# Performance work log

Measured on AMD Instinct MI355X. Metric: run time of the kernel, lower is better.

The kernel has to match this reference:

```python
import jax, jax.numpy as jnp
import numpy as np

N_NODES = 50000
N_EDGES = 1600000
IN_CH = 128
OUT_CH = 128


def setup_inputs() -> dict:
    key = jax.random.key(0)
    k1, k2, k3, k4, k5 = jax.random.split(key, 5)
    x = jax.random.normal(k1, (N_NODES, IN_CH), dtype=jnp.float32)
    # edge_index[0] = destination (row), edge_index[1] = source (col)
    edge_index = jax.random.randint(k2, (2, N_EDGES), 0, N_NODES, dtype=jnp.int64)
    # Linear parameters (PyTorch default init: U(-1/sqrt(fan_in), 1/sqrt(fan_in)))
    bound = 1.0 / np.sqrt(IN_CH)
    W = jax.random.uniform(k3, (OUT_CH, IN_CH), dtype=jnp.float32, minval=-bound, maxval=bound)
    b = jax.random.uniform(k4, (OUT_CH,), dtype=jnp.float32, minval=-bound, maxval=bound)
    return {"x": x, "edge_index": edge_index, "W": W, "b": b}


def reference(x, edge_index, W, b) -> jnp.ndarray:
    # Linear projection: h = x @ W^T + b  -> [N, OUT_CH]
    h = jnp.einsum("nd,od->no", x, W) + b
    # spmm sum aggregation: out[dst] = sum_{edges e: dst(e)=dst} h[src(e)]
    dst = edge_index[0]
    src = edge_index[1]
    out = jax.ops.segment_sum(h[src], dst, num_segments=N_NODES)
    return out
```

## Files before the change

kernel.cpp:

```cpp
#include <hip/hip_runtime.h>

constexpr int N  = 50000;
constexpr int E  = 1600000;
constexpr int CH = 128;

constexpr int BSZ  = 64;
constexpr int NB   = (N + BSZ - 1) / BSZ;
constexpr int CAP  = 2560;
constexpr int PBLK = 256;
constexpr int EPB  = E / PBLK;
constexpr int GEMM_BLOCKS = N / 16;

constexpr size_t H_OFF     = 0;
constexpr size_t H_SZ      = (size_t)N * CH * 2;
constexpr size_t PAIRS_OFF = H_OFF + H_SZ;
constexpr size_t PAIRS_SZ  = (size_t)NB * CAP * 4;
constexpr size_t GCUR_OFF  = PAIRS_OFF + PAIRS_SZ;
constexpr size_t GCUR_SZ   = 3328;
constexpr size_t REQUIRED  = GCUR_OFF + GCUR_SZ;
constexpr size_t FB_REQUIRED = H_SZ;

static __device__ __forceinline__ ushort f2bf(float f) {
    unsigned u = __float_as_uint(f);
    return (ushort)((u + 0x7fffu + ((u >> 16) & 1u)) >> 16);
}
static __device__ __forceinline__ float bf_lo(unsigned u) { return __uint_as_float(u << 16); }
static __device__ __forceinline__ float bf_hi(unsigned u) { return __uint_as_float(u & 0xffff0000u); }

typedef __attribute__((ext_vector_type(8))) short bf16x8;
typedef __attribute__((ext_vector_type(4))) float f32x4;

static __device__ __forceinline__ void gemm_body(int gb, int tid,
                                                 const float* __restrict__ x,
                                                 const float* __restrict__ W,
                                                 const float* __restrict__ bias,
                                                 ushort* __restrict__ h) {
    const int m    = tid & 15;
    const int q    = (tid >> 4) & 3;
    const int wave = tid >> 6;
    const int r0   = gb * 16;
    const int c0   = wave * 32;

    const float* xrow = x + (size_t)(r0 + m) * CH + q * 8;
    const float* wr0  = W + (size_t)(c0 + m) * CH + q * 8;
    const float* wr1  = wr0 + 16 * CH;

    f32x4 acc0 = {0.f, 0.f, 0.f, 0.f};
    f32x4 acc1 = {0.f, 0.f, 0.f, 0.f};

#pragma unroll
    for (int kc = 0; kc < CH; kc += 32) {
        float4 xa = *(const float4*)(xrow + kc);
        float4 xb = *(const float4*)(xrow + kc + 4);
        float4 wa0 = *(const float4*)(wr0 + kc);
        float4 wb0 = *(const float4*)(wr0 + kc + 4);
        float4 wa1 = *(const float4*)(wr1 + kc);
        float4 wb1 = *(const float4*)(wr1 + kc + 4);
        bf16x8 a, b0, b1;
        a[0] = (short)f2bf(xa.x); a[1] = (short)f2bf(xa.y);
        a[2] = (short)f2bf(xa.z); a[3] = (short)f2bf(xa.w);
        a[4] = (short)f2bf(xb.x); a[5] = (short)f2bf(xb.y);
        a[6] = (short)f2bf(xb.z); a[7] = (short)f2bf(xb.w);
        b0[0] = (short)f2bf(wa0.x); b0[1] = (short)f2bf(wa0.y);
        b0[2] = (short)f2bf(wa0.z); b0[3] = (short)f2bf(wa0.w);
        b0[4] = (short)f2bf(wb0.x); b0[5] = (short)f2bf(wb0.y);
        b0[6] = (short)f2bf(wb0.z); b0[7] = (short)f2bf(wb0.w);
        b1[0] = (short)f2bf(wa1.x); b1[1] = (short)f2bf(wa1.y);
        b1[2] = (short)f2bf(wa1.z); b1[3] = (short)f2bf(wa1.w);
        b1[4] = (short)f2bf(wb1.x); b1[5] = (short)f2bf(wb1.y);
        b1[6] = (short)f2bf(wb1.z); b1[7] = (short)f2bf(wb1.w);
        acc0 = __builtin_amdgcn_mfma_f32_16x16x32_bf16(a, b0, acc0, 0, 0, 0);
        acc1 = __builtin_amdgcn_mfma_f32_16x16x32_bf16(a, b1, acc1, 0, 0, 0);
    }

    const int col0 = c0 + m;
    const float bb0 = bias[col0];
    const float bb1 = bias[col0 + 16];
#pragma unroll
    for (int r = 0; r < 4; r++) {
        size_t row = (size_t)(r0 + q * 4 + r) * CH;
        h[row + col0]      = f2bf(acc0[r] + bb0);
        h[row + col0 + 16] = f2bf(acc1[r] + bb1);
    }
}

__global__ __launch_bounds__(256) void gemm_and_scatter(const float* __restrict__ x,
                                                        const float* __restrict__ W,
                                                        const float* __restrict__ bias,
                                                        ushort* __restrict__ h,
                                                        const int* __restrict__ ei,
                                                        int* __restrict__ gcur,
                                                        unsigned* __restrict__ pairs) {
    __shared__ unsigned raw[EPB];
    __shared__ ushort   srt16[EPB];
    __shared__ int cnt[NB];
    __shared__ int lstart[NB];
    __shared__ int gpos[NB];
    __shared__ int cur[NB];
    __shared__ int ssum[256];
    const int bid = blockIdx.x;
    const int tid = threadIdx.x;

    if (bid >= PBLK) {
        gemm_body(bid - PBLK, tid, x, W, bias, h);
        return;
    }

    const int k = bid;
    const int* dp = ei + k * EPB;
    const int* sp = ei + E + k * EPB;

    for (int j = tid; j < NB; j += 256) cnt[j] = 0;
    for (int i = tid; i < EPB; i += 256) {
        int d = dp[i], s = sp[i];
        raw[i] = ((unsigned)(d >> 6) << 22) | ((unsigned)(d & (BSZ - 1)) << 16) | (unsigned)s;
    }
    __syncthreads();

    for (int i = tid; i < EPB; i += 256) atomicAdd(&cnt[raw[i] >> 22], 1);
    __syncthreads();

    for (int j = tid; j < NB; j += 256) {
        int c = cnt[j];
        gpos[j] = j * CAP + (c ? atomicAdd(&gcur[j], c) : 0);
    }

    {
        const int base = tid * 4;
        int s = 0;
#pragma unroll
        for (int i = 0; i < 4; i++) { int j = base + i; if (j < NB) s += cnt[j]; }
        ssum[tid] = s;
        __syncthreads();
        for (int o = 1; o < 256; o <<= 1) {
            int u = (tid >= o) ? ssum[tid - o] : 0;
            __syncthreads();
            ssum[tid] += u;
            __syncthreads();
        }
        int run = ssum[tid] - s;
#pragma unroll
        for (int i = 0; i < 4; i++) {
            int j = base + i;
            if (j < NB) { lstart[j] = run; cur[j] = run; run += cnt[j]; }
        }
    }
    __syncthreads();

    for (int i = tid; i < EPB; i += 256) {
        int p = atomicAdd(&cur[raw[i] >> 22], 1);
        srt16[p] = (ushort)i;
    }
    __syncthreads();

    for (int i = tid; i < EPB; i += 256) {
        unsigned w = raw[srt16[i]];
        int bkt = w >> 22;
        int gdst = gpos[bkt] + (i - lstart[bkt]);
        if (gdst < (bkt + 1) * CAP)
            pairs[gdst] = w;
    }
}

__global__ __launch_bounds__(512) void agg_fused(const ushort* __restrict__ h,
                                                 const unsigned* __restrict__ pairs,
                                                 const int* __restrict__ gcur,
                                                 float* __restrict__ out) {
    __shared__ unsigned raw[CAP];
    __shared__ ushort   srt[CAP];
    __shared__ int hist[BSZ], offs[BSZ], cur[BSZ];
    const int b = blockIdx.x, t = threadIdx.x;
    const int cnt = min(gcur[b], CAP);
    const int wave = t >> 6;
    const int lane = t & 63;
    const int quarter = lane >> 4;
    const int cq      = lane & 15;

    const unsigned* slab = pairs + (size_t)b * CAP;
    for (int i = t; i < cnt; i += 512) raw[i] = slab[i];
    if (t < BSZ) hist[t] = 0;
    __syncthreads();
    for (int i = t; i < cnt; i += 512) atomicAdd(&hist[(raw[i] >> 16) & (BSZ - 1)], 1);
    __syncthreads();
    int v = (t < BSZ) ? hist[t] : 0;
    if (t < BSZ) offs[t] = v;
    __syncthreads();
    for (int o = 1; o < BSZ; o <<= 1) {
        int u = 0;
        if (t < BSZ && t >= o) u = offs[t - o];
        __syncthreads();
        if (t < BSZ) offs[t] += u;
        __syncthreads();
    }
    if (t < BSZ) { int excl = offs[t] - v; offs[t] = excl; cur[t] = excl; }
    __syncthreads();
    for (int i = t; i < cnt; i += 512) {
        unsigned w = raw[i];
        int p = atomicAdd(&cur[(w >> 16) & (BSZ - 1)], 1);
        srt[p] = (ushort)(w & 0xffffu);
    }
    __syncthreads();

    const ushort* hp = h + (size_t)cq * 8;

#pragma unroll
    for (int j = 0; j < 8; j++) {
        const int nl = wave * 8 + j;
        const int st = offs[nl];
        const int c  = hist[nl];
        float a0 = 0.f, a1 = 0.f, a2 = 0.f, a3 = 0.f;
        float a4 = 0.f, a5 = 0.f, a6 = 0.f, a7 = 0.f;
        int i = 0;
        for (; i + 16 <= c; i += 16) {
            const int e0 = st + i + quarter;
            int s0 = srt[e0];
            int s1 = srt[e0 + 4];
            int s2 = srt[e0 + 8];
            int s3 = srt[e0 + 12];
            uint4 v0 = *(const uint4*)(hp + (size_t)s0 * CH);
            uint4 v1 = *(const uint4*)(hp + (size_t)s1 * CH);
            uint4 v2 = *(const uint4*)(hp + (size_t)s2 * CH);
            uint4 v3 = *(const uint4*)(hp + (size_t)s3 * CH);
            a0 += bf_lo(v0.x); a1 += bf_hi(v0.x); a2 += bf_lo(v0.y); a3 += bf_hi(v0.y);
            a4 += bf_lo(v0.z); a5 += bf_hi(v0.z); a6 += bf_lo(v0.w); a7 += bf_hi(v0.w);
            a0 += bf_lo(v1.x); a1 += bf_hi(v1.x); a2 += bf_lo(v1.y); a3 += bf_hi(v1.y);
            a4 += bf_lo(v1.z); a5 += bf_hi(v1.z); a6 += bf_lo(v1.w); a7 += bf_hi(v1.w);
            a0 += bf_lo(v2.x); a1 += bf_hi(v2.x); a2 += bf_lo(v2.y); a3 += bf_hi(v2.y);
            a4 += bf_lo(v2.z); a5 += bf_hi(v2.z); a6 += bf_lo(v2.w); a7 += bf_hi(v2.w);
            a0 += bf_lo(v3.x); a1 += bf_hi(v3.x); a2 += bf_lo(v3.y); a3 += bf_hi(v3.y);
            a4 += bf_lo(v3.z); a5 += bf_hi(v3.z); a6 += bf_lo(v3.w); a7 += bf_hi(v3.w);
        }
        for (; i < c; i += 4) {
            if (i + quarter < c) {
                int s = srt[st + i + quarter];
                uint4 vv = *(const uint4*)(hp + (size_t)s * CH);
                a0 += bf_lo(vv.x); a1 += bf_hi(vv.x); a2 += bf_lo(vv.y); a3 += bf_hi(vv.y);
                a4 += bf_lo(vv.z); a5 += bf_hi(vv.z); a6 += bf_lo(vv.w); a7 += bf_hi(vv.w);
            }
        }
        a0 += __shfl_xor(a0, 16); a0 += __shfl_xor(a0, 32);
        a1 += __shfl_xor(a1, 16); a1 += __shfl_xor(a1, 32);
        a2 += __shfl_xor(a2, 16); a2 += __shfl_xor(a2, 32);
        a3 += __shfl_xor(a3, 16); a3 += __shfl_xor(a3, 32);
        a4 += __shfl_xor(a4, 16); a4 += __shfl_xor(a4, 32);
        a5 += __shfl_xor(a5, 16); a5 += __shfl_xor(a5, 32);
        a6 += __shfl_xor(a6, 16); a6 += __shfl_xor(a6, 32);
        a7 += __shfl_xor(a7, 16); a7 += __shfl_xor(a7, 32);
        const int n = b * BSZ + nl;
        if (quarter == 0 && n < N) {
            float* op = out + (size_t)n * CH + cq * 8;
            *(float4*)(op)     = make_float4(a0, a1, a2, a3);
            *(float4*)(op + 4) = make_float4(a4, a5, a6, a7);
        }
    }
}

__global__ __launch_bounds__(256) void gemm_only(const float* __restrict__ x,
                                                 const float* __restrict__ W,
                                                 const float* __restrict__ bias,
                                                 ushort* __restrict__ h) {
    gemm_body(blockIdx.x, threadIdx.x, x, W, bias, h);
}

__global__ void atomic_agg(const ushort* __restrict__ h, const int* __restrict__ ei,
                           float* __restrict__ out) {
    int tid = blockIdx.x * blockDim.x + threadIdx.x;
    int e  = tid >> 5;
    int cg = (tid & 31) * 4;
    if (e < E) {
        int d = ei[e];
        int s = ei[E + e];
        ushort4 v = *(const ushort4*)(h + (size_t)s * CH + cg);
        float* o = out + (size_t)d * CH + cg;
        atomicAdd(o + 0, __uint_as_float((unsigned)v.x << 16));
        atomicAdd(o + 1, __uint_as_float((unsigned)v.y << 16));
        atomicAdd(o + 2, __uint_as_float((unsigned)v.z << 16));
        atomicAdd(o + 3, __uint_as_float((unsigned)v.w << 16));
    }
}

extern "C" void kernel_launch(void* const* d_in, const int* in_sizes, int n_in,
                              void* d_out, int out_size, void* d_ws, size_t ws_size,
                              hipStream_t stream) {
    const float* x  = (const float*)d_in[0];
    const int*   ei = (const int*)d_in[1];
    const float* W  = (const float*)d_in[2];
    const float* b  = (const float*)d_in[3];
    float* out = (float*)d_out;

    char* ws = (char*)d_ws;
    ushort* h = (ushort*)(ws + H_OFF);

    if (ws_size >= REQUIRED) {
        unsigned* pairs = (unsigned*)(ws + PAIRS_OFF);
        int*      gcur  = (int*)(ws + GCUR_OFF);

        hipMemsetAsync(gcur, 0, NB * sizeof(int), stream);
        gemm_and_scatter<<<PBLK + GEMM_BLOCKS, 256, 0, stream>>>(x, W, b, h, ei, gcur, pairs);
        agg_fused<<<NB, 512, 0, stream>>>(h, pairs, gcur, out);
    } else if (ws_size >= FB_REQUIRED) {
        gemm_only<<<GEMM_BLOCKS, 256, 0, stream>>>(x, W, b, h);
        hipMemsetAsync(out, 0, (size_t)out_size * sizeof(float), stream);
        int total = E * 32;
        atomic_agg<<<(total + 255) / 256, 256, 0, stream>>>(h, ei, out);
    }
}
```

Measured before the change: 180.6 us.

## Pad per-node edge lists with zero sentinel row and gather eight rows per step

The aggregation kernel now rounds each node's edge count up to a multiple of 32 and fills the padding with a sentinel index that points at an extra all-zero row appended to h. This removes the remainder loop and its branches, and lets each quarter-wave issue eight independent gathers per iteration to raise memory-level parallelism. The cost is wasted gathers of the zero row, which average about 16 padded slots per node. Separately, both kernels fold histogram counting into the load loop and replace barrier-heavy shared-memory scans with wave shuffle scans.

```diff
diff --git a/kernel.cpp b/kernel.cpp
--- a/kernel.cpp
+++ b/kernel.cpp
@@ -7,12 +7,13 @@
 constexpr int BSZ  = 64;
 constexpr int NB   = (N + BSZ - 1) / BSZ;
 constexpr int CAP  = 2560;
+constexpr int SRTCAP = CAP + BSZ * 31 + 64;
 constexpr int PBLK = 256;
 constexpr int EPB  = E / PBLK;
 constexpr int GEMM_BLOCKS = N / 16;
 
 constexpr size_t H_OFF     = 0;
-constexpr size_t H_SZ      = (size_t)N * CH * 2;
+constexpr size_t H_SZ      = (size_t)(N + 1) * CH * 2;
 constexpr size_t PAIRS_OFF = H_OFF + H_SZ;
 constexpr size_t PAIRS_SZ  = (size_t)NB * CAP * 4;
 constexpr size_t GCUR_OFF  = PAIRS_OFF + PAIRS_SZ;
@@ -97,7 +98,7 @@
     __shared__ int lstart[NB];
     __shared__ int gpos[NB];
     __shared__ int cur[NB];
-    __shared__ int ssum[256];
+    __shared__ int wsum[4];
     const int bid = blockIdx.x;
     const int tid = threadIdx.x;
 
@@ -110,14 +111,16 @@
     const int* dp = ei + k * EPB;
     const int* sp = ei + E + k * EPB;
 
+    if (bid == 0 && tid < 64) ((unsigned*)(h + (size_t)N * CH))[tid] = 0u;
+
     for (int j = tid; j < NB; j += 256) cnt[j] = 0;
+    __syncthreads();
     for (int i = tid; i < EPB; i += 256) {
         int d = dp[i], s = sp[i];
-        raw[i] = ((unsigned)(d >> 6) << 22) | ((unsigned)(d & (BSZ - 1)) << 16) | (unsigned)s;
-    }
-    __syncthreads();
-
-    for (int i = tid; i < EPB; i += 256) atomicAdd(&cnt[raw[i] >> 22], 1);
+        unsigned w = ((unsigned)(d >> 6) << 22) | ((unsigned)(d & (BSZ - 1)) << 16) | (unsigned)s;
+        raw[i] = w;
+        atomicAdd(&cnt[w >> 22], 1);
+    }
     __syncthreads();
 
     for (int j = tid; j < NB; j += 256) {
@@ -130,15 +133,18 @@
         int s = 0;
 #pragma unroll
         for (int i = 0; i < 4; i++) { int j = base + i; if (j < NB) s += cnt[j]; }
-        ssum[tid] = s;
+        const int lane = tid & 63;
+        const int wid  = tid >> 6;
+        int incl = s;
+#pragma unroll
+        for (int o = 1; o < 64; o <<= 1) {
+            int u = __shfl_up(incl, o);
+            if (lane >= o) incl += u;
+        }
+        if (lane == 63) wsum[wid] = incl;
         __syncthreads();
-        for (int o = 1; o < 256; o <<= 1) {
-            int u = (tid >= o) ? ssum[tid - o] : 0;
-            __syncthreads();
-            ssum[tid] += u;
-            __syncthreads();
-        }
-        int run = ssum[tid] - s;
+        int run = incl - s;
+        for (int w = 0; w < wid; w++) run += wsum[w];
 #pragma unroll
         for (int i = 0; i < 4; i++) {
             int j = base + i;
@@ -167,8 +173,8 @@
                                                  const int* __restrict__ gcur,
                                                  float* __restrict__ out) {
     __shared__ unsigned raw[CAP];
-    __shared__ ushort   srt[CAP];
-    __shared__ int hist[BSZ], offs[BSZ], cur[BSZ];
+    __shared__ ushort   srt[SRTCAP];
+    __shared__ int hist[BSZ], offs[BSZ], cur[BSZ], cpad[BSZ];
     const int b = blockIdx.x, t = threadIdx.x;
     const int cnt = min(gcur[b], CAP);
     const int wave = t >> 6;
@@ -176,23 +182,34 @@
     const int quarter = lane >> 4;
     const int cq      = lane & 15;
 
+    if (t < BSZ) hist[t] = 0;
+    __syncthreads();
+
     const unsigned* slab = pairs + (size_t)b * CAP;
-    for (int i = t; i < cnt; i += 512) raw[i] = slab[i];
-    if (t < BSZ) hist[t] = 0;
-    __syncthreads();
-    for (int i = t; i < cnt; i += 512) atomicAdd(&hist[(raw[i] >> 16) & (BSZ - 1)], 1);
-    __syncthreads();
-    int v = (t < BSZ) ? hist[t] : 0;
-    if (t < BSZ) offs[t] = v;
-    __syncthreads();
-    for (int o = 1; o < BSZ; o <<= 1) {
-        int u = 0;
-        if (t < BSZ && t >= o) u = offs[t - o];
-        __syncthreads();
-        if (t < BSZ) offs[t] += u;
-        __syncthreads();
-    }
-    if (t < BSZ) { int excl = offs[t] - v; offs[t] = excl; cur[t] = excl; }
+    for (int i = t; i < cnt; i += 512) {
+        unsigned w = slab[i];
+        raw[i] = w;
+        atomicAdd(&hist[(w >> 16) & (BSZ - 1)], 1);
+    }
+    __syncthreads();
+
+    if (t < BSZ) {
+        int c  = hist[t];
+        int cp = (c + 31) & ~31;
+        int incl = cp;
+#pragma unroll
+        for (int o = 1; o < 64; o <<= 1) {
+            int u = __shfl_up(incl, o);
+            if (lane >= o) incl += u;
+        }
+        offs[t] = incl - cp;
+        cur[t]  = incl - cp;
+        cpad[t] = cp;
+    }
+    __syncthreads();
+
+    const int tot = offs[BSZ - 1] + cpad[BSZ - 1];
+    for (int i = t; i < tot; i += 512) srt[i] = (ushort)N;
     __syncthreads();
     for (int i = t; i < cnt; i += 512) {
         unsigned w = raw[i];
@@ -203,24 +220,31 @@
 
     const ushort* hp = h + (size_t)cq * 8;
 
-#pragma unroll
+#pragma unroll 1
     for (int j = 0; j < 8; j++) {
         const int nl = wave * 8 + j;
         const int st = offs[nl];
-        const int c  = hist[nl];
+        const int cp = cpad[nl];
         float a0 = 0.f, a1 = 0.f, a2 = 0.f, a3 = 0.f;
         float a4 = 0.f, a5 = 0.f, a6 = 0.f, a7 = 0.f;
-        int i = 0;
-        for (; i + 16 <= c; i += 16) {
+        for (int i = 0; i < cp; i += 32) {
             const int e0 = st + i + quarter;
-            int s0 = srt[e0];
-            int s1 = srt[e0 + 4];
-            int s2 = srt[e0 + 8];
-            int s3 = srt[e0 + 12];
+            const int s0 = srt[e0];
+            const int s1 = srt[e0 + 4];
+            const int s2 = srt[e0 + 8];
+            const int s3 = srt[e0 + 12];
+            const int s4 = srt[e0 + 16];
+            const int s5 = srt[e0 + 20];
+            const int s6 = srt[e0 + 24];
+            const int s7 = srt[e0 + 28];
             uint4 v0 = *(const uint4*)(hp + (size_t)s0 * CH);
             uint4 v1 = *(const uint4*)(hp + (size_t)s1 * CH);
             uint4 v2 = *(const uint4*)(hp + (size_t)s2 * CH);
             uint4 v3 = *(const uint4*)(hp + (size_t)s3 * CH);
+            uint4 v4 = *(const uint4*)(hp + (size_t)s4 * CH);
+            uint4 v5 = *(const uint4*)(hp + (size_t)s5 * CH);
+            uint4 v6 = *(const uint4*)(hp + (size_t)s6 * CH);
+            uint4 v7 = *(const uint4*)(hp + (size_t)s7 * CH);
             a0 += bf_lo(v0.x); a1 += bf_hi(v0.x); a2 += bf_lo(v0.y); a3 += bf_hi(v0.y);
             a4 += bf_lo(v0.z); a5 += bf_hi(v0.z); a6 += bf_lo(v0.w); a7 += bf_hi(v0.w);
             a0 += bf_lo(v1.x); a1 += bf_hi(v1.x); a2 += bf_lo(v1.y); a3 += bf_hi(v1.y);
@@ -229,14 +253,14 @@
             a4 += bf_lo(v2.z); a5 += bf_hi(v2.z); a6 += bf_lo(v2.w); a7 += bf_hi(v2.w);
             a0 += bf_lo(v3.x); a1 += bf_hi(v3.x); a2 += bf_lo(v3.y); a3 += bf_hi(v3.y);
             a4 += bf_lo(v3.z); a5 += bf_hi(v3.z); a6 += bf_lo(v3.w); a7 += bf_hi(v3.w);
-        }
-        for (; i < c; i += 4) {
-            if (i + quarter < c) {
-                int s = srt[st + i + quarter];
-                uint4 vv = *(const uint4*)(hp + (size_t)s * CH);
-                a0 += bf_lo(vv.x); a1 += bf_hi(vv.x); a2 += bf_lo(vv.y); a3 += bf_hi(vv.y);
-                a4 += bf_lo(vv.z); a5 += bf_hi(vv.z); a6 += bf_lo(vv.w); a7 += bf_hi(vv.w);
-            }
+            a0 += bf_lo(v4.x); a1 += bf_hi(v4.x); a2 += bf_lo(v4.y); a3 += bf_hi(v4.y);
+            a4 += bf_lo(v4.z); a5 += bf_hi(v4.z); a6 += bf_lo(v4.w); a7 += bf_hi(v4.w);
+            a0 += bf_lo(v5.x); a1 += bf_hi(v5.x); a2 += bf_lo(v5.y); a3 += bf_hi(v5.y);
+            a4 += bf_lo(v5.z); a5 += bf_hi(v5.z); a6 += bf_lo(v5.w); a7 += bf_hi(v5.w);
+            a0 += bf_lo(v6.x); a1 += bf_hi(v6.x); a2 += bf_lo(v6.y); a3 += bf_hi(v6.y);
+            a4 += bf_lo(v6.z); a5 += bf_hi(v6.z); a6 += bf_lo(v6.w); a7 += bf_hi(v6.w);
+            a0 += bf_lo(v7.x); a1 += bf_hi(v7.x); a2 += bf_lo(v7.y); a3 += bf_hi(v7.y);
+            a4 += bf_lo(v7.z); a5 += bf_hi(v7.z); a6 += bf_lo(v7.w); a7 += bf_hi(v7.w);
         }
         a0 += __shfl_xor(a0, 16); a0 += __shfl_xor(a0, 32);
         a1 += __shfl_xor(a1, 16); a1 += __shfl_xor(a1, 32);
```

Measured after the change: 177.9 us. About the same (-1.5%).
